# Optimization experiments

Hardware: AMD Instinct MI355X
Metric: run time of the kernel (lower is better)

Reference implementation:

```python
import jax, jax.numpy as jnp
import numpy as np
from jax import lax

B, T, F, H, NC = 64, 256, 64, 128, 2


def setup_inputs() -> dict:
    key = jax.random.key(0)
    ks = jax.random.split(key, 10)
    # timestamps: sorted ints with duplicates -> exercises per-timestamp mean aggregation
    t = jnp.sort(jax.random.randint(ks[0], (B, T), 0, T // 2), axis=1).astype(jnp.float32)
    m = jax.random.randint(ks[1], (B, T), 0, F).astype(jnp.float32)
    x = jax.random.normal(ks[2], (B, T), dtype=jnp.float32)
    delt = jax.random.uniform(ks[3], (B, T), dtype=jnp.float32)
    X = jnp.stack([t, m, x, delt], axis=1)  # [B, 4, T]
    lengths = jax.random.randint(ks[4], (B,), T // 2, T + 1).astype(jnp.int32)
    s = 1.0 / np.sqrt(H + 1)
    W_lin = jax.random.uniform(ks[5], (F, H + 1, 4 * H), minval=-s, maxval=s, dtype=jnp.float32)
    b_lin = jax.random.uniform(ks[6], (F, 4 * H), minval=-s, maxval=s, dtype=jnp.float32)
    W_dec = jax.random.uniform(ks[7], (F,), minval=-1.0, maxval=1.0, dtype=jnp.float32)
    b_dec = jax.random.uniform(ks[8], (F,), minval=-1.0, maxval=1.0, dtype=jnp.float32)
    so = 1.0 / np.sqrt(F * H + H)
    k9, k10 = jax.random.split(ks[9])
    W_out = jax.random.uniform(k9, (F * H + H, NC), minval=-so, maxval=so, dtype=jnp.float32)
    b_out = jax.random.uniform(k10, (NC,), minval=-so, maxval=so, dtype=jnp.float32)
    return {"X": X, "lengths": lengths, "W_lin": W_lin, "b_lin": b_lin,
            "W_dec": W_dec, "b_dec": b_dec, "W_out": W_out, "b_out": b_out}


def _forward(X, lengths, W_lin, b_lin, W_dec, b_dec, W_out, b_out):
    nF, Hp1, H4 = W_lin.shape
    hs = Hp1 - 1
    t = X[:, 0]
    m = X[:, 1].astype(jnp.int32)
    x = X[:, 2]
    delt = X[:, 3]
    idx = jnp.arange(t.shape[1])
    valid = idx[None, :] < lengths[:, None]                       # event is real
    t_next = jnp.concatenate([t[:, 1:], t[:, -1:] + 1.0], axis=1)
    # last event of a consecutive-equal-timestamp group (within valid length)
    boundary = (idx[None, :] == (lengths[:, None] - 1)) | (t_next != t)

    def per_sample(m_s, x_s, d_s, v_s, b_s):
        def step(carry, inp):
            h_t, c_t, acc, cnt = carry
            mj, xj, dj, vj, bj = inp
            # feature-specific decay of that feature's hidden row
            dm = W_dec[mj] * dj + b_dec[mj]
            decay = jnp.exp(-jnp.maximum(0.0, dm))
            h_dec = decay * h_t[mj]
            inp_vec = jnp.concatenate([xj[None], h_dec])          # [H+1]
            gates = inp_vec @ W_lin[mj] + b_lin[mj]               # [4H]
            gi, gf, go, gc = jnp.split(gates, 4)
            c_cand = jax.nn.sigmoid(gf) * c_t + jax.nn.sigmoid(gi) * jnp.tanh(gc)
            h_row = jax.nn.sigmoid(go) * jnp.tanh(c_cand)
            h_t = jnp.where(vj, h_t.at[mj].set(h_row), h_t)
            acc = acc + jnp.where(vj, c_cand, 0.0)
            cnt = cnt + jnp.where(vj, 1.0, 0.0)
            close = vj & bj                                       # end of timestamp group
            c_t = jnp.where(close, acc / jnp.maximum(cnt, 1.0), c_t)
            acc = jnp.where(close, jnp.zeros_like(acc), acc)
            cnt = jnp.where(close, 0.0, cnt)
            return (h_t, c_t, acc, cnt), None

        init = (jnp.zeros((nF, hs), jnp.float32), jnp.zeros((hs,), jnp.float32),
                jnp.zeros((hs,), jnp.float32), jnp.float32(0.0))
        (h_t, c_t, _, _), _ = lax.scan(step, init, (m_s, x_s, d_s, v_s, b_s))
        feats = jnp.concatenate([c_t, h_t.reshape(-1)])           # [H + F*H]
        return jax.nn.softmax(feats @ W_out + b_out)

    return jax.vmap(per_sample)(m, x, delt, valid, boundary)      # [B, n_class]


def reference(X, lengths, W_lin, b_lin, W_dec, b_dec, W_out, b_out):
    return _forward(X, lengths, W_lin, b_lin, W_dec, b_dec, W_out, b_out)
```

## Files before the change

kernel.cpp:

```cpp
#include <hip/hip_runtime.h>
#include <math.h>

#define BATCH 64
#define T 256
#define NF 64
#define H 128
#define H4 512
#define HP1 129
#define WF_STRIDE (HP1 * H4)
#define FEATS (NF * H + H)
#define NTHREADS 512
#define PACK_UINT4_PER_F 8192
#define PACK_BYTES (64u * PACK_UINT4_PER_F * 16u)

typedef _Float16 half2_t __attribute__((ext_vector_type(2)));

__device__ __forceinline__ float sigmoidf_(float x) {
    return 1.0f / (1.0f + __expf(-x));
}

__device__ __forceinline__ float tanhf_(float x) {
    float ax = fabsf(x);
    float e = __expf(2.0f * ax);
    float r = 1.0f - 2.0f / (e + 1.0f);
    return copysignf(r, x);
}

__device__ __forceinline__ float fdot2_(half2_t a, half2_t b, float c) {
#if defined(__has_builtin)
#if __has_builtin(__builtin_amdgcn_fdot2)
    return __builtin_amdgcn_fdot2(a, b, c, false);
#else
    return fmaf((float)a.x, (float)b.x, fmaf((float)a.y, (float)b.y, c));
#endif
#else
    return fmaf((float)a.x, (float)b.x, fmaf((float)a.y, (float)b.y, c));
#endif
}

__global__ __launch_bounds__(256)
void repack_kernel(const float* __restrict__ W_lin, uint4* __restrict__ pack) {
    const int lin = blockIdx.x * 256 + threadIdx.x;
    const int f   = lin >> 13;
    const int i   = (lin >> 9) & 15;
    const int tid = lin & 511;
    const int kq  = tid >> 7;
    const int g4  = tid & 127;
    const int k0  = kq * 32 + 2 * i;
    const float* src = W_lin + (size_t)f * WF_STRIDE + (size_t)(1 + k0) * H4 + 4 * g4;
    const float4 r0 = *(const float4*)(src);
    const float4 r1 = *(const float4*)(src + H4);
    half2_t h[4];
    h[0].x = (_Float16)r0.x; h[0].y = (_Float16)r1.x;
    h[1].x = (_Float16)r0.y; h[1].y = (_Float16)r1.y;
    h[2].x = (_Float16)r0.z; h[2].y = (_Float16)r1.z;
    h[3].x = (_Float16)r0.w; h[3].y = (_Float16)r1.w;
    pack[lin] = *(uint4*)h;
}

__global__ __launch_bounds__(NTHREADS, 2)
void lstm_scan_fp16_kernel(const float* __restrict__ X,
                           const int* __restrict__ lengths,
                           const float* __restrict__ W_lin,
                           const float* __restrict__ b_lin,
                           const float* __restrict__ W_dec,
                           const float* __restrict__ b_dec,
                           const float* __restrict__ W_out,
                           const float* __restrict__ b_out,
                           const uint4* __restrict__ pack,
                           float* __restrict__ out)
{
    __shared__ float s_feats[FEATS];
    __shared__ half2_t s_inp2[H / 2];
    __shared__ float s_part[4][H4];
    __shared__ float s_X[4 * T];
    __shared__ float s_wdec[NF];
    __shared__ float s_bdec[NF];
    __shared__ float s_red[16];

    float* s_ct = s_feats;
    float* s_ht = s_feats + H;

    const int tid = threadIdx.x;
    const int b   = blockIdx.x;
    const int g4  = tid & 127;
    const int kq  = tid >> 7;

    const float* Xb = X + b * 4 * T;
    const int len = lengths[b];

    for (int i = tid; i < NF * H; i += NTHREADS) s_ht[i] = 0.0f;
    for (int i = tid; i < 4 * T; i += NTHREADS) s_X[i] = Xb[i];
    if (tid < NF) { s_wdec[tid] = W_dec[tid]; s_bdec[tid] = b_dec[tid]; }
    if (tid < H / 2) { half2_t z; z.x = (_Float16)0.0f; z.y = (_Float16)0.0f; s_inp2[tid] = z; }
    __syncthreads();

    float c_t = 0.0f, acc = 0.0f, cnt = 0.0f;

    uint4 bufA[16], bufB[16];
    float4 blA = make_float4(0.f, 0.f, 0.f, 0.f), blB = make_float4(0.f, 0.f, 0.f, 0.f);
    float4 wxA = make_float4(0.f, 0.f, 0.f, 0.f), wxB = make_float4(0.f, 0.f, 0.f, 0.f);

    {
        const int m0 = (int)s_X[T];
        const uint4* Wp = pack + m0 * PACK_UINT4_PER_F + tid;
        #pragma unroll
        for (int i = 0; i < 16; ++i) bufA[i] = Wp[i * 512];
        if (tid < H) {
            const float* bb = b_lin + m0 * H4 + tid;
            blA.x = bb[0]; blA.y = bb[H]; blA.z = bb[2 * H]; blA.w = bb[3 * H];
        }
        if (kq == 0) wxA = *(const float4*)(W_lin + (size_t)m0 * WF_STRIDE + 4 * g4);
    }

    #define STEP(CURW, NXTW, CURB, NXTB, CURX, NXTX)                                \
    {                                                                               \
        const int   mj = (int)s_X[T + j];                                           \
        const float xj = s_X[2 * T + j];                                            \
        const int   jn = (j + 1 < T) ? (j + 1) : (T - 1);                           \
        const int   mjn = (int)s_X[T + jn];                                         \
              \
        {                                                                           \
            const uint4* Wp = pack + mjn * PACK_UINT4_PER_F + tid;                  \
            _Pragma("unroll")                                                       \
            for (int i = 0; i < 16; ++i) NXTW[i] = Wp[i * 512];                     \
        }                                                                           \
        if (tid < H) {                                                              \
            const float* bb = b_lin + mjn * H4 + tid;                               \
            NXTB.x = bb[0]; NXTB.y = bb[H]; NXTB.z = bb[2 * H]; NXTB.w = bb[3 * H]; \
        }                                                                           \
        if (kq == 0) NXTX = *(const float4*)(W_lin + (size_t)mjn * WF_STRIDE + 4 * g4); \
                                     \
        float a0 = 0.0f, a1 = 0.0f, a2 = 0.0f, a3 = 0.0f;                           \
        _Pragma("unroll")                                                           \
        for (int i = 0; i < 16; ++i) {                                              \
            union { uint4 u; half2_t h[4]; } cv;                                    \
            cv.u = CURW[i];                                                         \
            const half2_t iv = s_inp2[kq * 16 + i];                                 \
            a0 = fdot2_(cv.h[0], iv, a0);                                           \
            a1 = fdot2_(cv.h[1], iv, a1);                                           \
            a2 = fdot2_(cv.h[2], iv, a2);                                           \
            a3 = fdot2_(cv.h[3], iv, a3);                                           \
        }                                                                           \
        if (kq == 0) {                                                              \
            a0 = fmaf(xj, CURX.x, a0); a1 = fmaf(xj, CURX.y, a1);                   \
            a2 = fmaf(xj, CURX.z, a2); a3 = fmaf(xj, CURX.w, a3);                   \
        }                                                                           \
        float4 a4; a4.x = a0; a4.y = a1; a4.z = a2; a4.w = a3;                      \
        *(float4*)(&s_part[kq][4 * g4]) = a4;                                       \
        __syncthreads();                                     \
        if (tid < H) {                                                              \
            const int h = tid;                                                      \
            const float gi = s_part[0][h]         + s_part[1][h]         + s_part[2][h]         + s_part[3][h]         + CURB.x; \
            const float gf = s_part[0][H + h]     + s_part[1][H + h]     + s_part[2][H + h]     + s_part[3][H + h]     + CURB.y; \
            const float go = s_part[0][2*H + h]   + s_part[1][2*H + h]   + s_part[2][2*H + h]   + s_part[3][2*H + h]   + CURB.z; \
            const float gc = s_part[0][3*H + h]   + s_part[1][3*H + h]   + s_part[2][3*H + h]   + s_part[3][3*H + h]   + CURB.w; \
            const float c_cand = sigmoidf_(gf) * c_t + sigmoidf_(gi) * tanhf_(gc);  \
            const float h_row  = sigmoidf_(go) * tanhf_(c_cand);                    \
            s_ht[mj * H + h] = h_row;                                               \
            acc += c_cand;                                                          \
            cnt += 1.0f;                                                            \
            const float tj = s_X[j];                                                \
            const float tn = (j < T - 1) ? s_X[j + 1] : (tj + 1.0f);                \
            const bool boundary = (j == len - 1) || (tn != tj);                     \
            if (boundary) { c_t = acc / fmaxf(cnt, 1.0f); acc = 0.0f; cnt = 0.0f; } \
                                      \
            const float dn  = s_X[3 * T + jn];                                      \
            const float dmn = fmaf(s_wdec[mjn], dn, s_bdec[mjn]);                   \
            const float den = __expf(-fmaxf(0.0f, dmn));                            \
            const float hv  = (mjn == mj) ? h_row : s_ht[mjn * H + h];              \
            ((_Float16*)s_inp2)[h] = (_Float16)(den * hv);                          \
        }                                                                           \
        __syncthreads();                                 \
    }

    int j = 0;
    while (j < len) {
        STEP(bufA, bufB, blA, blB, wxA, wxB); ++j;
        if (j >= len) break;
        STEP(bufB, bufA, blB, blA, wxB, wxA); ++j;
    }
    #undef STEP

    if (tid < H) s_ct[tid] = c_t;
    __syncthreads();

    float z0 = 0.0f, z1 = 0.0f;
    for (int i = tid; i < FEATS; i += NTHREADS) {
        const float f = s_feats[i];
        const float2 w = *(const float2*)(W_out + 2 * i);
        z0 = fmaf(f, w.x, z0);
        z1 = fmaf(f, w.y, z1);
    }
    #pragma unroll
    for (int off = 32; off > 0; off >>= 1) {
        z0 += __shfl_down(z0, off, 64);
        z1 += __shfl_down(z1, off, 64);
    }
    const int wave = tid >> 6, lane = tid & 63;
    if (lane == 0) { s_red[2 * wave] = z0; s_red[2 * wave + 1] = z1; }
    __syncthreads();
    if (tid == 0) {
        float a0 = b_out[0], a1 = b_out[1];
        #pragma unroll
        for (int w = 0; w < 8; ++w) { a0 += s_red[2 * w]; a1 += s_red[2 * w + 1]; }
        const float mx = fmaxf(a0, a1);
        const float e0 = __expf(a0 - mx), e1 = __expf(a1 - mx);
        const float inv = 1.0f / (e0 + e1);
        out[2 * b]     = e0 * inv;
        out[2 * b + 1] = e1 * inv;
    }
}

__global__ __launch_bounds__(NTHREADS)
void lstm_scan_kernel(const float* __restrict__ X,
                      const int* __restrict__ lengths,
                      const float* __restrict__ W_lin,
                      const float* __restrict__ b_lin,
                      const float* __restrict__ W_dec,
                      const float* __restrict__ b_dec,
                      const float* __restrict__ W_out,
                      const float* __restrict__ b_out,
                      float* __restrict__ out)
{
    __shared__ float s_feats[FEATS];
    __shared__ float s_inp[H];
    __shared__ float s_part[4][H4];
    __shared__ float s_X[4 * T];
    __shared__ float s_wdec[NF];
    __shared__ float s_bdec[NF];
    __shared__ float s_red[16];

    float* s_ct = s_feats;
    float* s_ht = s_feats + H;

    const int tid = threadIdx.x;
    const int b   = blockIdx.x;
    const int g4  = tid & 127;
    const int kq  = tid >> 7;

    const float* Xb = X + b * 4 * T;
    const int len = lengths[b];

    for (int i = tid; i < NF * H; i += NTHREADS) s_ht[i] = 0.0f;
    for (int i = tid; i < 4 * T; i += NTHREADS) s_X[i] = Xb[i];
    if (tid < NF) { s_wdec[tid] = W_dec[tid]; s_bdec[tid] = b_dec[tid]; }
    __syncthreads();

    float c_t = 0.0f, acc = 0.0f, cnt = 0.0f;

    for (int j = 0; j < len; ++j) {
        const int   mj = (int)s_X[T + j];
        const float xj = s_X[2 * T + j];
        const float* Wf = W_lin + mj * WF_STRIDE;

        float bl0, bl1, bl2, bl3;
        if (tid < H) {
            const float dj    = s_X[3 * T + j];
            const float dm    = fmaf(s_wdec[mj], dj, s_bdec[mj]);
            const float decay = __expf(-fmaxf(0.0f, dm));
            s_inp[tid] = decay * s_ht[mj * H + tid];
            const int m4 = mj * H4;
            bl0 = b_lin[m4 + tid];
            bl1 = b_lin[m4 + H + tid];
            bl2 = b_lin[m4 + 2 * H + tid];
            bl3 = b_lin[m4 + 3 * H + tid];
        }
        __syncthreads();

        float4 a4 = make_float4(0.0f, 0.0f, 0.0f, 0.0f);
        {
            const float*  wr  = Wf + (1 + kq * 32) * H4 + 4 * g4;
            const float4* ivp = (const float4*)(s_inp + kq * 32);
            #pragma unroll
            for (int c = 0; c < 8; ++c) {
                const float4 v = ivp[c];
                const float* wrc = wr + (4 * c) * H4;
                const float4 w0 = *(const float4*)(wrc);
                const float4 w1 = *(const float4*)(wrc + H4);
                const float4 w2 = *(const float4*)(wrc + 2 * H4);
                const float4 w3 = *(const float4*)(wrc + 3 * H4);
                a4.x = fmaf(v.x, w0.x, a4.x); a4.y = fmaf(v.x, w0.y, a4.y);
                a4.z = fmaf(v.x, w0.z, a4.z); a4.w = fmaf(v.x, w0.w, a4.w);
                a4.x = fmaf(v.y, w1.x, a4.x); a4.y = fmaf(v.y, w1.y, a4.y);
                a4.z = fmaf(v.y, w1.z, a4.z); a4.w = fmaf(v.y, w1.w, a4.w);
                a4.x = fmaf(v.z, w2.x, a4.x); a4.y = fmaf(v.z, w2.y, a4.y);
                a4.z = fmaf(v.z, w2.z, a4.z); a4.w = fmaf(v.z, w2.w, a4.w);
                a4.x = fmaf(v.w, w3.x, a4.x); a4.y = fmaf(v.w, w3.y, a4.y);
                a4.z = fmaf(v.w, w3.z, a4.z); a4.w = fmaf(v.w, w3.w, a4.w);
            }
        }
        if (kq == 0) {
            const float4 w = *(const float4*)(Wf + 4 * g4);
            a4.x = fmaf(xj, w.x, a4.x); a4.y = fmaf(xj, w.y, a4.y);
            a4.z = fmaf(xj, w.z, a4.z); a4.w = fmaf(xj, w.w, a4.w);
        }
        *(float4*)(&s_part[kq][4 * g4]) = a4;
        __syncthreads();

        if (tid < H) {
            const int h = tid;
            const float gi = s_part[0][h]         + s_part[1][h]         + s_part[2][h]         + s_part[3][h]         + bl0;
            const float gf = s_part[0][H + h]     + s_part[1][H + h]     + s_part[2][H + h]     + s_part[3][H + h]     + bl1;
            const float go = s_part[0][2*H + h]   + s_part[1][2*H + h]   + s_part[2][2*H + h]   + s_part[3][2*H + h]   + bl2;
            const float gc = s_part[0][3*H + h]   + s_part[1][3*H + h]   + s_part[2][3*H + h]   + s_part[3][3*H + h]   + bl3;

            const float c_cand = sigmoidf_(gf) * c_t + sigmoidf_(gi) * tanhf_(gc);
            const float h_row  = sigmoidf_(go) * tanhf_(c_cand);
            s_ht[mj * H + h] = h_row;
            acc += c_cand;
            cnt += 1.0f;

            const float tj = s_X[j];
            const float tn = (j < T - 1) ? s_X[j + 1] : (tj + 1.0f);
            const bool boundary = (j == len - 1) || (tn != tj);
            if (boundary) { c_t = acc / fmaxf(cnt, 1.0f); acc = 0.0f; cnt = 0.0f; }
        }
        __syncthreads();
    }

    if (tid < H) s_ct[tid] = c_t;
    __syncthreads();

    float z0 = 0.0f, z1 = 0.0f;
    for (int i = tid; i < FEATS; i += NTHREADS) {
        const float f = s_feats[i];
        const float2 w = *(const float2*)(W_out + 2 * i);
        z0 = fmaf(f, w.x, z0);
        z1 = fmaf(f, w.y, z1);
    }
    #pragma unroll
    for (int off = 32; off > 0; off >>= 1) {
        z0 += __shfl_down(z0, off, 64);
        z1 += __shfl_down(z1, off, 64);
    }
    const int wave = tid >> 6, lane = tid & 63;
    if (lane == 0) { s_red[2 * wave] = z0; s_red[2 * wave + 1] = z1; }
    __syncthreads();
    if (tid == 0) {
        float a0 = b_out[0], a1 = b_out[1];
        #pragma unroll
        for (int w = 0; w < 8; ++w) { a0 += s_red[2 * w]; a1 += s_red[2 * w + 1]; }
        const float mx = fmaxf(a0, a1);
        const float e0 = __expf(a0 - mx), e1 = __expf(a1 - mx);
        const float inv = 1.0f / (e0 + e1);
        out[2 * b]     = e0 * inv;
        out[2 * b + 1] = e1 * inv;
    }
}

extern "C" void kernel_launch(void* const* d_in, const int* in_sizes, int n_in,
                              void* d_out, int out_size, void* d_ws, size_t ws_size,
                              hipStream_t stream) {
    const float* X      = (const float*)d_in[0];
    const int*   lens   = (const int*)d_in[1];
    const float* W_lin  = (const float*)d_in[2];
    const float* b_lin  = (const float*)d_in[3];
    const float* W_dec  = (const float*)d_in[4];
    const float* b_dec  = (const float*)d_in[5];
    const float* W_out  = (const float*)d_in[6];
    const float* b_out  = (const float*)d_in[7];
    float* out = (float*)d_out;

    if (ws_size >= (size_t)PACK_BYTES) {
        uint4* pack = (uint4*)d_ws;
        hipLaunchKernelGGL(repack_kernel, dim3(2048), dim3(256), 0, stream, W_lin, pack);
        hipLaunchKernelGGL(lstm_scan_fp16_kernel, dim3(BATCH), dim3(NTHREADS), 0, stream,
                           X, lens, W_lin, b_lin, W_dec, b_dec, W_out, b_out, pack, out);
    } else {
        hipLaunchKernelGGL(lstm_scan_kernel, dim3(BATCH), dim3(NTHREADS), 0, stream,
                           X, lens, W_lin, b_lin, W_dec, b_dec, W_out, b_out, out);
    }
}
```

Baseline: 525.4 us.

## Double block size to 1024 threads and split gate matvec into two K halves

The scan kernel now runs 1024 threads per block. Each thread owns one gate column and half of the hidden dimension, replacing the previous layout of 4 columns by a quarter of K. The fp16 repack is rearranged to match: column-major per thread with 8 K-rows per uint4. Per-thread register buffers halve, which is meant to cut per-step latency through more parallel loads and a shorter 2-way reduction. The cost is more threads contending at each per-step barrier, and scalar global loads in the repack.

```diff
diff --git a/kernel.cpp b/kernel.cpp
--- a/kernel.cpp
+++ b/kernel.cpp
@@ -9,7 +9,7 @@
 #define HP1 129
 #define WF_STRIDE (HP1 * H4)
 #define FEATS (NF * H + H)
-#define NTHREADS 512
+#define NTH 1024
 #define PACK_UINT4_PER_F 8192
 #define PACK_BYTES (64u * PACK_UINT4_PER_F * 16u)
 
@@ -42,23 +42,22 @@
 void repack_kernel(const float* __restrict__ W_lin, uint4* __restrict__ pack) {
     const int lin = blockIdx.x * 256 + threadIdx.x;
     const int f   = lin >> 13;
-    const int i   = (lin >> 9) & 15;
-    const int tid = lin & 511;
-    const int kq  = tid >> 7;
-    const int g4  = tid & 127;
-    const int k0  = kq * 32 + 2 * i;
-    const float* src = W_lin + (size_t)f * WF_STRIDE + (size_t)(1 + k0) * H4 + 4 * g4;
-    const float4 r0 = *(const float4*)(src);
-    const float4 r1 = *(const float4*)(src + H4);
+    const int i   = (lin >> 10) & 7;
+    const int tid = lin & 1023;
+    const int kh  = tid >> 9;
+    const int c   = tid & 511;
+    const int k0  = kh * 64 + i * 8;
+    const float* src = W_lin + (size_t)f * WF_STRIDE + (size_t)(1 + k0) * H4 + c;
     half2_t h[4];
-    h[0].x = (_Float16)r0.x; h[0].y = (_Float16)r1.x;
-    h[1].x = (_Float16)r0.y; h[1].y = (_Float16)r1.y;
-    h[2].x = (_Float16)r0.z; h[2].y = (_Float16)r1.z;
-    h[3].x = (_Float16)r0.w; h[3].y = (_Float16)r1.w;
+    #pragma unroll
+    for (int r = 0; r < 4; ++r) {
+        h[r].x = (_Float16)src[(2 * r) * H4];
+        h[r].y = (_Float16)src[(2 * r + 1) * H4];
+    }
     pack[lin] = *(uint4*)h;
 }
 
-__global__ __launch_bounds__(NTHREADS, 2)
+__global__ __launch_bounds__(NTH, 4)
 void lstm_scan_fp16_kernel(const float* __restrict__ X,
                            const int* __restrict__ lengths,
                            const float* __restrict__ W_lin,
@@ -72,45 +71,45 @@
 {
     __shared__ float s_feats[FEATS];
     __shared__ half2_t s_inp2[H / 2];
-    __shared__ float s_part[4][H4];
+    __shared__ float s_part[2][H4];
     __shared__ float s_X[4 * T];
     __shared__ float s_wdec[NF];
     __shared__ float s_bdec[NF];
-    __shared__ float s_red[16];
+    __shared__ float s_red[32];
 
     float* s_ct = s_feats;
     float* s_ht = s_feats + H;
 
     const int tid = threadIdx.x;
     const int b   = blockIdx.x;
-    const int g4  = tid & 127;
-    const int kq  = tid >> 7;
+    const int c   = tid & 511;
+    const int kh  = tid >> 9;
 
     const float* Xb = X + b * 4 * T;
     const int len = lengths[b];
 
-    for (int i = tid; i < NF * H; i += NTHREADS) s_ht[i] = 0.0f;
-    for (int i = tid; i < 4 * T; i += NTHREADS) s_X[i] = Xb[i];
+    for (int i = tid; i < NF * H; i += NTH) s_ht[i] = 0.0f;
+    for (int i = tid; i < 4 * T; i += NTH) s_X[i] = Xb[i];
     if (tid < NF) { s_wdec[tid] = W_dec[tid]; s_bdec[tid] = b_dec[tid]; }
     if (tid < H / 2) { half2_t z; z.x = (_Float16)0.0f; z.y = (_Float16)0.0f; s_inp2[tid] = z; }
     __syncthreads();
 
     float c_t = 0.0f, acc = 0.0f, cnt = 0.0f;
 
-    uint4 bufA[16], bufB[16];
+    uint4 bufA[8], bufB[8];
     float4 blA = make_float4(0.f, 0.f, 0.f, 0.f), blB = make_float4(0.f, 0.f, 0.f, 0.f);
-    float4 wxA = make_float4(0.f, 0.f, 0.f, 0.f), wxB = make_float4(0.f, 0.f, 0.f, 0.f);
+    float  wxA = 0.0f, wxB = 0.0f;
 
     {
         const int m0 = (int)s_X[T];
         const uint4* Wp = pack + m0 * PACK_UINT4_PER_F + tid;
         #pragma unroll
-        for (int i = 0; i < 16; ++i) bufA[i] = Wp[i * 512];
+        for (int i = 0; i < 8; ++i) bufA[i] = Wp[i * NTH];
         if (tid < H) {
             const float* bb = b_lin + m0 * H4 + tid;
             blA.x = bb[0]; blA.y = bb[H]; blA.z = bb[2 * H]; blA.w = bb[3 * H];
         }
-        if (kq == 0) wxA = *(const float4*)(W_lin + (size_t)m0 * WF_STRIDE + 4 * g4);
+        if (kh == 0) wxA = W_lin[(size_t)m0 * WF_STRIDE + c];
     }
 
     #define STEP(CURW, NXTW, CURB, NXTB, CURX, NXTX)                                \
@@ -123,38 +122,35 @@
         {                                                                           \
             const uint4* Wp = pack + mjn * PACK_UINT4_PER_F + tid;                  \
             _Pragma("unroll")                                                       \
-            for (int i = 0; i < 16; ++i) NXTW[i] = Wp[i * 512];                     \
+            for (int i = 0; i < 8; ++i) NXTW[i] = Wp[i * NTH];                      \
         }                                                                           \
         if (tid < H) {                                                              \
             const float* bb = b_lin + mjn * H4 + tid;                               \
             NXTB.x = bb[0]; NXTB.y = bb[H]; NXTB.z = bb[2 * H]; NXTB.w = bb[3 * H]; \
         }                                                                           \
-        if (kq == 0) NXTX = *(const float4*)(W_lin + (size_t)mjn * WF_STRIDE + 4 * g4); \
+        if (kh == 0) NXTX = W_lin[(size_t)mjn * WF_STRIDE + c];                     \
                                      \
-        float a0 = 0.0f, a1 = 0.0f, a2 = 0.0f, a3 = 0.0f;                           \
+        float a0 = 0.0f, a1 = 0.0f;                                                 \
         _Pragma("unroll")                                                           \
-        for (int i = 0; i < 16; ++i) {                                              \
+        for (int i = 0; i < 8; ++i) {                                               \
             union { uint4 u; half2_t h[4]; } cv;                                    \
             cv.u = CURW[i];                                                         \
-            const half2_t iv = s_inp2[kq * 16 + i];                                 \
-            a0 = fdot2_(cv.h[0], iv, a0);                                           \
-            a1 = fdot2_(cv.h[1], iv, a1);                                           \
-            a2 = fdot2_(cv.h[2], iv, a2);                                           \
-            a3 = fdot2_(cv.h[3], iv, a3);                                           \
+            const int ib = (kh << 5) + (i << 2);                                    \
+            a0 = fdot2_(cv.h[0], s_inp2[ib],     a0);                               \
+            a1 = fdot2_(cv.h[1], s_inp2[ib + 1], a1);                               \
+            a0 = fdot2_(cv.h[2], s_inp2[ib + 2], a0);                               \
+            a1 = fdot2_(cv.h[3], s_inp2[ib + 3], a1);                               \
         }                                                                           \
-        if (kq == 0) {                                                              \
-            a0 = fmaf(xj, CURX.x, a0); a1 = fmaf(xj, CURX.y, a1);                   \
-            a2 = fmaf(xj, CURX.z, a2); a3 = fmaf(xj, CURX.w, a3);                   \
-        }                                                                           \
-        float4 a4; a4.x = a0; a4.y = a1; a4.z = a2; a4.w = a3;                      \
-        *(float4*)(&s_part[kq][4 * g4]) = a4;                                       \
+        float a = a0 + a1;                                                          \
+        if (kh == 0) a = fmaf(xj, CURX, a);                                         \
+        s_part[kh][c] = a;                                                          \
         __syncthreads();                                     \
         if (tid < H) {                                                              \
             const int h = tid;                                                      \
-            const float gi = s_part[0][h]         + s_part[1][h]         + s_part[2][h]         + s_part[3][h]         + CURB.x; \
-            const float gf = s_part[0][H + h]     + s_part[1][H + h]     + s_part[2][H + h]     + s_part[3][H + h]     + CURB.y; \
-            const float go = s_part[0][2*H + h]   + s_part[1][2*H + h]   + s_part[2][2*H + h]   + s_part[3][2*H + h]   + CURB.z; \
-            const float gc = s_part[0][3*H + h]   + s_part[1][3*H + h]   + s_part[2][3*H + h]   + s_part[3][3*H + h]   + CURB.w; \
+            const float gi = s_part[0][h]       + s_part[1][h]       + CURB.x;      \
+            const float gf = s_part[0][H + h]   + s_part[1][H + h]   + CURB.y;      \
+            const float go = s_part[0][2*H + h] + s_part[1][2*H + h] + CURB.z;      \
+            const float gc = s_part[0][3*H + h] + s_part[1][3*H + h] + CURB.w;      \
             const float c_cand = sigmoidf_(gf) * c_t + sigmoidf_(gi) * tanhf_(gc);  \
             const float h_row  = sigmoidf_(go) * tanhf_(c_cand);                    \
             s_ht[mj * H + h] = h_row;                                               \
@@ -186,7 +182,7 @@
     __syncthreads();
 
     float z0 = 0.0f, z1 = 0.0f;
-    for (int i = tid; i < FEATS; i += NTHREADS) {
+    for (int i = tid; i < FEATS; i += NTH) {
         const float f = s_feats[i];
         const float2 w = *(const float2*)(W_out + 2 * i);
         z0 = fmaf(f, w.x, z0);
@@ -203,7 +199,7 @@
     if (tid == 0) {
         float a0 = b_out[0], a1 = b_out[1];
         #pragma unroll
-        for (int w = 0; w < 8; ++w) { a0 += s_red[2 * w]; a1 += s_red[2 * w + 1]; }
+        for (int w = 0; w < 16; ++w) { a0 += s_red[2 * w]; a1 += s_red[2 * w + 1]; }
         const float mx = fmaxf(a0, a1);
         const float e0 = __expf(a0 - mx), e1 = __expf(a1 - mx);
         const float inv = 1.0f / (e0 + e1);
@@ -212,6 +208,7 @@
     }
 }
 
+#define NTHREADS 512
 __global__ __launch_bounds__(NTHREADS)
 void lstm_scan_kernel(const float* __restrict__ X,
                       const int* __restrict__ lengths,
@@ -365,7 +362,7 @@
     if (ws_size >= (size_t)PACK_BYTES) {
         uint4* pack = (uint4*)d_ws;
         hipLaunchKernelGGL(repack_kernel, dim3(2048), dim3(256), 0, stream, W_lin, pack);
-        hipLaunchKernelGGL(lstm_scan_fp16_kernel, dim3(BATCH), dim3(NTHREADS), 0, stream,
+        hipLaunchKernelGGL(lstm_scan_fp16_kernel, dim3(BATCH), dim3(NTH), 0, stream,
                            X, lens, W_lin, b_lin, W_dec, b_dec, W_out, b_out, pack, out);
     } else {
         hipLaunchKernelGGL(lstm_scan_kernel, dim3(BATCH), dim3(NTHREADS), 0, stream,
```

After: 500.2 us. -4.8%, faster.
